# Kernel tuning notes

Measured on AMD Instinct MI355X. Metric: run time of the kernel, lower is better.

## Reference

```python
import jax, jax.numpy as jnp
import numpy as np

N = 65536
R = 9          # num_relations + 1
D_IN = 256
D_HID = 512
D_OUT = 256
N_HIDDEN = 2


def _xavier(key, shape):
    fan_out, fan_in = shape[-2], shape[-1]
    limit = np.sqrt(6.0 / (fan_in + fan_out))
    return jax.random.uniform(key, shape, jnp.float32, -limit, limit)


def setup_inputs() -> dict:
    key = jax.random.key(0)
    ks = jax.random.split(key, 12)
    inp = {
        "x": jax.random.normal(ks[0], (N, D_IN), jnp.float32),
        "edge_attr": jax.random.uniform(ks[1], (N, R), jnp.float32),
    }
    dims = [(D_HID, D_IN)] + [(D_HID, D_HID)] * N_HIDDEN + [(D_OUT, D_HID)]
    for i, (o, ii) in enumerate(dims):
        inp[f"W{i}"] = _xavier(ks[2 + 2 * i], (R, o, ii))
        inp[f"b{i}"] = _xavier(ks[3 + 2 * i], (R, o))
    return inp


def _linear_kg(x, edge_attr, W, b):
    # roi,ni,nr->no : relation-mixed linear per node
    y = jnp.einsum("roi,ni,nr->no", W, x, edge_attr)
    return y + edge_attr @ b


def reference(x, edge_attr, W0, b0, W1, b1, W2, b2, W3, b3):
    y = jax.nn.relu(_linear_kg(x, edge_attr, W0, b0))
    y = jax.nn.relu(_linear_kg(y, edge_attr, W1, b1))
    y = jax.nn.relu(_linear_kg(y, edge_attr, W2, b2))
    y = _linear_kg(y, edge_attr, W3, b3)
    return y
```

## Files before the change

### kernel.cpp

```cpp
#include <hip/hip_runtime.h>
#include <stdint.h>

using f32x4  = __attribute__((ext_vector_type(4))) float;
using bf16x8 = __attribute__((ext_vector_type(8))) __bf16;

#define GLOAD_LDS16(src, dst) __builtin_amdgcn_global_load_lds(                 \
    (const __attribute__((address_space(1))) void*)(src),                      \
    (__attribute__((address_space(3))) void*)(dst), 16, 0, 0)


__global__ void cvt_x_kernel(const float* __restrict__ x, __bf16* __restrict__ out) {
    const int u    = blockIdx.x * 256 + threadIdx.x;
    const int lane = u & 63;
    const int f    = (u >> 6) & 31;
    const int c    = (u >> 11) & 1;
    const int rb   = u >> 12;
    const int row  = rb * 128 + ((f >> 2) << 4) + (lane & 15);
    const int i    = c * 128 + ((f & 3) << 5) + ((lane >> 4) << 3);
    const float4 a = *(const float4*)(x + (size_t)row * 256 + i);
    const float4 b = *(const float4*)(x + (size_t)row * 256 + i + 4);
    bf16x8 pv;
    pv[0] = (__bf16)a.x; pv[1] = (__bf16)a.y; pv[2] = (__bf16)a.z; pv[3] = (__bf16)a.w;
    pv[4] = (__bf16)b.x; pv[5] = (__bf16)b.y; pv[6] = (__bf16)b.z; pv[7] = (__bf16)b.w;
    *(bf16x8*)(out + (size_t)u * 8) = pv;
}

template<int I, int O>
__global__ void prep_w_kernel(const float* __restrict__ W, __bf16* __restrict__ Bt) {
    constexpr int NCH = I >> 7;
    const int u    = blockIdx.x * 256 + threadIdx.x;
    const int r    = blockIdx.y;
    const int nb   = blockIdx.z;
    const int lane = u & 63;
    const int g    = (u >> 6) & 15;
    const int h    = (u >> 10) & 1;
    const int c    = u >> 11;
    const int mi   = g >> 1;
    const int ks   = (h << 1) + (g & 1);
    const int row  = nb * 128 + mi * 16 + (lane & 15);
    const int i    = c * 128 + ks * 32 + ((lane >> 4) << 3);
    const float* src = W + ((size_t)r * O + row) * I + i;
    const float4 a = *(const float4*)src;
    const float4 b = *(const float4*)(src + 4);
    bf16x8 pv;
    pv[0] = (__bf16)a.x; pv[1] = (__bf16)a.y; pv[2] = (__bf16)a.z; pv[3] = (__bf16)a.w;
    pv[4] = (__bf16)b.x; pv[5] = (__bf16)b.y; pv[6] = (__bf16)b.z; pv[7] = (__bf16)b.w;
    *(bf16x8*)(Bt + ((((size_t)nb * 9 + r) * NCH + c) * 2048 + (u & 2047)) * 8) = pv;
}

template<int O>
__global__ void prep_bias_kernel(const float* __restrict__ b, __bf16* __restrict__ BtB) {
    const int u    = blockIdx.x * 256 + threadIdx.x;
    const int nb   = u >> 10;
    const int q    = u & 1023;
    const int lane = q & 63;
    const int f    = q >> 6;
    const int row  = nb * 128 + ((f >> 1) << 4) + (lane & 15);
    const int kb   = ((f & 1) << 5) + ((lane >> 4) << 3);
    bf16x8 pv;
#pragma unroll
    for (int e = 0; e < 8; ++e) {
        const int k = kb + e;
        pv[e] = (k < 9) ? (__bf16)b[(size_t)k * O + row] : (__bf16)0.f;
    }
    *(bf16x8*)(BtB + (size_t)u * 8) = pv;
}

template<int I, int O, bool RELU, bool OUTF32>
__global__ __launch_bounds__(256, 2)
void kg_gemm(const __bf16* __restrict__ A, const float* __restrict__ E,
             const __bf16* __restrict__ Bt, const __bf16* __restrict__ BtB,
             void* __restrict__ Outv) {
    constexpr int NCH = I >> 7;
    constexpr int NBN = O >> 7;
    static_assert((I & 127) == 0 && (O & 127) == 0, "tile divisibility");

    __shared__ __align__(16) char lds[65536 + 4608];
    float* const ldsE = (float*)(lds + 65536);

    const int tid  = threadIdx.x;
    const int nwg  = gridDim.x;
    const int braw = blockIdx.x;
    const int bid  = (braw & 7) * (nwg >> 3) + (braw >> 3);
    const int rb   = bid / NBN;
    const int nb   = bid % NBN;
    const int bm0  = rb << 7;
    const int bn0  = nb << 7;
    const int lane = tid & 63;
    const int wid  = tid >> 6;
    const int wr   = (wid >> 1) << 6;
    const int wc   = (wid & 1) << 6;
    const int l15  = lane & 15;
    const int lq   = lane >> 4;

    if (tid < 128) {
        const float* e = E + (size_t)(bm0 + tid) * 9;
#pragma unroll
        for (int q = 0; q < 9; ++q) ldsE[q * 128 + tid] = e[q];
    }
    asm volatile("s_waitcnt lgkmcnt(0)" ::: "memory");
    __builtin_amdgcn_s_barrier();

    f32x4 acc[4][4];
#pragma unroll
    for (int m = 0; m < 4; ++m)
#pragma unroll
        for (int n = 0; n < 4; ++n)
            acc[m][n] = f32x4{0.f, 0.f, 0.f, 0.f};
    const f32x4 zero4 = {0.f, 0.f, 0.f, 0.f};

    const size_t Bbase = (size_t)nb * 9 * NCH * 2048;
    const __bf16* Arb  = A + (size_t)rb * NCH * 2048 * 8;
    const int afb = (wr >> 4) << 2;
    const int g0  = (wc >> 4) << 1;
    char* const wlds = lds + (wid << 14);

    auto stageW = [&](int r2, int c2, int h2) {
        const __bf16* src = Bt + (Bbase + ((size_t)r2 * NCH + c2) * 2048
                                  + (h2 << 10) + (g0 << 6)) * 8;
        char* dst = wlds + (h2 << 13);
#pragma unroll
        for (int it = 0; it < 8; ++it) {
            const int q = it * 64 + lane;
            GLOAD_LDS16(src + (size_t)q * 8, dst + q * 16);
        }
    };

    bf16x8 af[4][4];
    stageW(0, 0, 0); stageW(0, 0, 1);

#pragma unroll 1
    for (int c = 0; c < NCH; ++c) {
#pragma unroll 1
        for (int r = 0; r < 9; ++r) {
            f32x4 acc2[4][4];
#pragma unroll
            for (int h = 0; h < 2; ++h) {
                const bool first = (r == 0) && (h == 0);
                const bool lastC = (c == NCH - 1);
                if (first) {
                    const __bf16* Ab = Arb + (size_t)c * 2048 * 8;
#pragma unroll
                    for (int m = 0; m < 4; ++m)
#pragma unroll
                        for (int ks = 0; ks < 4; ++ks)
                            af[m][ks] = *(const bf16x8*)(Ab + ((size_t)((afb + (m << 2) + ks) << 6) + lane) * 8);
                    asm volatile("s_waitcnt vmcnt(24)" ::: "memory");
                } else if (lastC && r == 8 && h == 1) {
                    asm volatile("s_waitcnt vmcnt(0)" ::: "memory");
                } else {
                    asm volatile("s_waitcnt vmcnt(8)" ::: "memory");
                }
                __builtin_amdgcn_sched_barrier(0);
                const char* bp = wlds + (h << 13);
                bf16x8 bv[4][2];
#pragma unroll
                for (int n = 0; n < 4; ++n)
#pragma unroll
                    for (int j = 0; j < 2; ++j)
                        bv[n][j] = *(const bf16x8*)(bp + ((((n << 1) + j) << 6) + lane) * 16);
                asm volatile("s_waitcnt lgkmcnt(0)" ::: "memory");
                __builtin_amdgcn_sched_barrier(0);
                if (!(lastC && r == 8))
                    stageW((r < 8) ? r + 1 : 0, (r < 8) ? c : c + 1, h);
                if (first) asm volatile("s_waitcnt vmcnt(8)" ::: "memory");
                __builtin_amdgcn_sched_barrier(0);
                __builtin_amdgcn_s_setprio(1);
#pragma unroll
                for (int j = 0; j < 2; ++j)
#pragma unroll
                    for (int m = 0; m < 4; ++m)
#pragma unroll
                        for (int n = 0; n < 4; ++n)
                            acc2[m][n] = __builtin_amdgcn_mfma_f32_16x16x32_bf16(
                                af[m][(h << 1) + j], bv[n][j],
                                (h == 0 && j == 0) ? zero4 : acc2[m][n], 0, 0, 0);
                __builtin_amdgcn_s_setprio(0);
            }
#pragma unroll
            for (int m = 0; m < 4; ++m) {
                const f32x4 ev = *(const f32x4*)(ldsE + r * 128 + wr + m * 16 + lq * 4);
#pragma unroll
                for (int n = 0; n < 4; ++n)
#pragma unroll
                    for (int j = 0; j < 4; ++j)
                        acc[m][n][j] += ev[j] * acc2[m][n][j];
            }
        }
    }

    __syncthreads();
    {
        char* const bufB = lds;
        char* const bufA = lds + 16384;
#pragma unroll
        for (int rr = 0; rr < 4; ++rr) {
            const int q = rr * 256 + tid;
            GLOAD_LDS16(BtB + ((size_t)nb * 1024 + q) * 8, bufB + q * 16);
        }
#pragma unroll
        for (int rr = 0; rr < 4; ++rr) {
            const int q    = rr * 256 + tid;
            const int ln   = q & 63;
            const int f    = q >> 6;
            const int row  = ((f >> 1) << 4) + (ln & 15);
            const int kb   = ((f & 1) << 5) + ((ln >> 4) << 3);
            bf16x8 pv;
#pragma unroll
            for (int e8 = 0; e8 < 8; ++e8) {
                const int k = kb + e8;
                pv[e8] = (k < 9) ? (__bf16)ldsE[k * 128 + row] : (__bf16)0.f;
            }
            *(bf16x8*)(bufA + q * 16) = pv;
        }
        __syncthreads();
#pragma unroll
        for (int ks = 0; ks < 2; ++ks) {
            bf16x8 av[4], bv[4];
#pragma unroll
            for (int m = 0; m < 4; ++m)
                av[m] = *(const bf16x8*)(bufA + (((((wr >> 4) + m) * 2 + ks) << 6) + lane) * 16);
#pragma unroll
            for (int n = 0; n < 4; ++n)
                bv[n] = *(const bf16x8*)(bufB + (((((wc >> 4) + n) * 2 + ks) << 6) + lane) * 16);
#pragma unroll
            for (int m = 0; m < 4; ++m)
#pragma unroll
                for (int n = 0; n < 4; ++n)
                    acc[m][n] = __builtin_amdgcn_mfma_f32_16x16x32_bf16(
                        av[m], bv[n], acc[m][n], 0, 0, 0);
        }
    }

    if (OUTF32) {
        const int orow0 = bm0 + wr + lq * 4;
        const int ocol0 = bn0 + wc + l15;
#pragma unroll
        for (int m = 0; m < 4; ++m)
#pragma unroll
            for (int n = 0; n < 4; ++n)
#pragma unroll
                for (int j = 0; j < 4; ++j) {
                    float v = acc[m][n][j];
                    if (RELU) v = fmaxf(v, 0.f);
                    ((float*)Outv)[(size_t)(orow0 + m * 16 + j) * O + (ocol0 + n * 16)] = v;
                }
    } else {
        constexpr int NCHn = O >> 7;
        __bf16* outp = (__bf16*)Outv;
#pragma unroll
        for (int m = 0; m < 4; ++m) {
#pragma unroll
            for (int n = 0; n < 4; ++n) {
                const int col  = bn0 + wc + n * 16 + l15;
                const int c2   = col >> 7;
                const int f2   = (((wr >> 4) + m) << 2) + ((col >> 5) & 3);
                const int ln2  = ((col >> 3) & 3) * 16 + lq * 4;
                const size_t base =
                    (((size_t)rb * NCHn + c2) * 2048 + f2 * 64 + ln2) * 8 + (col & 7);
#pragma unroll
                for (int j = 0; j < 4; ++j) {
                    float v = acc[m][n][j];
                    if (RELU) v = fmaxf(v, 0.f);
                    outp[base + (size_t)j * 8] = (__bf16)v;
                }
            }
        }
    }
}

extern "C" void kernel_launch(void* const* d_in, const int* in_sizes, int n_in,
                              void* d_out, int out_size, void* d_ws, size_t ws_size,
                              hipStream_t stream) {
    const float* x  = (const float*)d_in[0];
    const float* E  = (const float*)d_in[1];
    const float* W0 = (const float*)d_in[2];
    const float* b0 = (const float*)d_in[3];
    const float* W1 = (const float*)d_in[4];
    const float* b1 = (const float*)d_in[5];
    const float* W2 = (const float*)d_in[6];
    const float* b2 = (const float*)d_in[7];
    const float* W3 = (const float*)d_in[8];
    const float* b3 = (const float*)d_in[9];

    char* ws = (char*)d_ws;
    const size_t actBytes = (size_t)65536 * 512 * 2;
    __bf16* actA = (__bf16*)ws;
    __bf16* actB = (__bf16*)(ws + actBytes);
    char* p = ws + 2 * actBytes;
    __bf16* Bt0 = (__bf16*)p; p += (size_t)4 * 9 * 2 * 2048 * 16;
    __bf16* Bt1 = (__bf16*)p; p += (size_t)4 * 9 * 4 * 2048 * 16;
    __bf16* Bt2 = (__bf16*)p; p += (size_t)4 * 9 * 4 * 2048 * 16;
    __bf16* Bt3 = (__bf16*)p; p += (size_t)2 * 9 * 4 * 2048 * 16;
    __bf16* BtB0 = (__bf16*)p; p += (size_t)4 * 1024 * 16;
    __bf16* BtB1 = (__bf16*)p; p += (size_t)4 * 1024 * 16;
    __bf16* BtB2 = (__bf16*)p; p += (size_t)4 * 1024 * 16;
    __bf16* BtB3 = (__bf16*)p; p += (size_t)2 * 1024 * 16;
    if (ws_size < (size_t)(p - ws)) return;

    cvt_x_kernel<<<dim3(8192), dim3(256), 0, stream>>>(x, actA);
    prep_w_kernel<256, 512><<<dim3(16, 9, 4), dim3(256), 0, stream>>>(W0, Bt0);
    prep_w_kernel<512, 512><<<dim3(32, 9, 4), dim3(256), 0, stream>>>(W1, Bt1);
    prep_w_kernel<512, 512><<<dim3(32, 9, 4), dim3(256), 0, stream>>>(W2, Bt2);
    prep_w_kernel<512, 256><<<dim3(32, 9, 2), dim3(256), 0, stream>>>(W3, Bt3);
    prep_bias_kernel<512><<<dim3(16), dim3(256), 0, stream>>>(b0, BtB0);
    prep_bias_kernel<512><<<dim3(16), dim3(256), 0, stream>>>(b1, BtB1);
    prep_bias_kernel<512><<<dim3(16), dim3(256), 0, stream>>>(b2, BtB2);
    prep_bias_kernel<256><<<dim3(8),  dim3(256), 0, stream>>>(b3, BtB3);

    kg_gemm<256, 512, true,  false><<<dim3(2048), dim3(256), 0, stream>>>(actA, E, Bt0, BtB0, actB);
    kg_gemm<512, 512, true,  false><<<dim3(2048), dim3(256), 0, stream>>>(actB, E, Bt1, BtB1, actA);
    kg_gemm<512, 512, true,  false><<<dim3(2048), dim3(256), 0, stream>>>(actA, E, Bt2, BtB2, actB);
    kg_gemm<512, 256, false, true ><<<dim3(1024), dim3(256), 0, stream>>>(actB, E, Bt3, BtB3, d_out);
}
```

Before: 970.8 us.

## Fold per-relation scaling into each K-half and restart weight staging per chunk

Drops the acc2 intermediate that held the relation-r partial product across both K-halves. Each half's MFMA result is now scaled by the edge_attr coefficients and added into the main accumulator right away, which cuts register use at the cost of doing the VALU scaling twice per relation. Weight staging no longer prefetches across chunk boundaries: the A fragments and the first relation's weights are loaded at the start of each chunk. The s_setprio hints are removed, and the MFMA issue order is reorganised into independent chains of four. This may open a pipeline bubble at every chunk start in exchange for lower register pressure and simpler waitcnt logic.

```diff
diff --git a/kernel.cpp b/kernel.cpp
--- a/kernel.cpp
+++ b/kernel.cpp
@@ -112,12 +112,12 @@
     const size_t Bbase = (size_t)nb * 9 * NCH * 2048;
     const __bf16* Arb  = A + (size_t)rb * NCH * 2048 * 8;
     const int afb = (wr >> 4) << 2;
-    const int g0  = (wc >> 4) << 1;
+    const int G0  = (wid & 1) << 3;
     char* const wlds = lds + (wid << 14);
 
     auto stageW = [&](int r2, int c2, int h2) {
         const __bf16* src = Bt + (Bbase + ((size_t)r2 * NCH + c2) * 2048
-                                  + (h2 << 10) + (g0 << 6)) * 8;
+                                  + (h2 << 10) + (G0 << 6)) * 8;
         char* dst = wlds + (h2 << 13);
 #pragma unroll
         for (int it = 0; it < 8; ++it) {
@@ -127,30 +127,29 @@
     };
 
     bf16x8 af[4][4];
-    stageW(0, 0, 0); stageW(0, 0, 1);
 
 #pragma unroll 1
     for (int c = 0; c < NCH; ++c) {
+        asm volatile("s_waitcnt lgkmcnt(0)" ::: "memory");
+        __builtin_amdgcn_sched_barrier(0);
+        {
+            const __bf16* Ab = Arb + (size_t)c * 2048 * 8;
+#pragma unroll
+            for (int m = 0; m < 4; ++m)
+#pragma unroll
+                for (int ks = 0; ks < 4; ++ks)
+                    af[m][ks] = *(const bf16x8*)(Ab + ((size_t)((afb + (m << 2) + ks) << 6) + lane) * 8);
+        }
+        stageW(0, c, 0);
+        stageW(0, c, 1);
+
 #pragma unroll 1
         for (int r = 0; r < 9; ++r) {
-            f32x4 acc2[4][4];
 #pragma unroll
             for (int h = 0; h < 2; ++h) {
-                const bool first = (r == 0) && (h == 0);
-                const bool lastC = (c == NCH - 1);
-                if (first) {
-                    const __bf16* Ab = Arb + (size_t)c * 2048 * 8;
-#pragma unroll
-                    for (int m = 0; m < 4; ++m)
-#pragma unroll
-                        for (int ks = 0; ks < 4; ++ks)
-                            af[m][ks] = *(const bf16x8*)(Ab + ((size_t)((afb + (m << 2) + ks) << 6) + lane) * 8);
-                    asm volatile("s_waitcnt vmcnt(24)" ::: "memory");
-                } else if (lastC && r == 8 && h == 1) {
-                    asm volatile("s_waitcnt vmcnt(0)" ::: "memory");
-                } else {
-                    asm volatile("s_waitcnt vmcnt(8)" ::: "memory");
-                }
+                const int s = 2 * r + h;
+                if (s < 17) asm volatile("s_waitcnt vmcnt(8)" ::: "memory");
+                else        asm volatile("s_waitcnt vmcnt(0)" ::: "memory");
                 __builtin_amdgcn_sched_barrier(0);
                 const char* bp = wlds + (h << 13);
                 bf16x8 bv[4][2];
@@ -159,32 +158,33 @@
 #pragma unroll
                     for (int j = 0; j < 2; ++j)
                         bv[n][j] = *(const bf16x8*)(bp + ((((n << 1) + j) << 6) + lane) * 16);
-                asm volatile("s_waitcnt lgkmcnt(0)" ::: "memory");
-                __builtin_amdgcn_sched_barrier(0);
-                if (!(lastC && r == 8))
-                    stageW((r < 8) ? r + 1 : 0, (r < 8) ? c : c + 1, h);
-                if (first) asm volatile("s_waitcnt vmcnt(8)" ::: "memory");
-                __builtin_amdgcn_sched_barrier(0);
-                __builtin_amdgcn_s_setprio(1);
-#pragma unroll
-                for (int j = 0; j < 2; ++j)
-#pragma unroll
-                    for (int m = 0; m < 4; ++m)
-#pragma unroll
-                        for (int n = 0; n < 4; ++n)
-                            acc2[m][n] = __builtin_amdgcn_mfma_f32_16x16x32_bf16(
-                                af[m][(h << 1) + j], bv[n][j],
-                                (h == 0 && j == 0) ? zero4 : acc2[m][n], 0, 0, 0);
-                __builtin_amdgcn_s_setprio(0);
-            }
-#pragma unroll
-            for (int m = 0; m < 4; ++m) {
-                const f32x4 ev = *(const f32x4*)(ldsE + r * 128 + wr + m * 16 + lq * 4);
-#pragma unroll
-                for (int n = 0; n < 4; ++n)
-#pragma unroll
-                    for (int j = 0; j < 4; ++j)
-                        acc[m][n][j] += ev[j] * acc2[m][n][j];
+                f32x4 ev[4];
+#pragma unroll
+                for (int m = 0; m < 4; ++m)
+                    ev[m] = *(const f32x4*)(ldsE + r * 128 + wr + m * 16 + lq * 4);
+#pragma unroll
+                for (int n = 0; n < 4; ++n) {
+                    f32x4 t0 = __builtin_amdgcn_mfma_f32_16x16x32_bf16(af[0][2*h], bv[n][0], zero4, 0, 0, 0);
+                    f32x4 t1 = __builtin_amdgcn_mfma_f32_16x16x32_bf16(af[1][2*h], bv[n][0], zero4, 0, 0, 0);
+                    f32x4 t2 = __builtin_amdgcn_mfma_f32_16x16x32_bf16(af[2][2*h], bv[n][0], zero4, 0, 0, 0);
+                    f32x4 t3 = __builtin_amdgcn_mfma_f32_16x16x32_bf16(af[3][2*h], bv[n][0], zero4, 0, 0, 0);
+                    t0 = __builtin_amdgcn_mfma_f32_16x16x32_bf16(af[0][2*h+1], bv[n][1], t0, 0, 0, 0);
+                    t1 = __builtin_amdgcn_mfma_f32_16x16x32_bf16(af[1][2*h+1], bv[n][1], t1, 0, 0, 0);
+                    t2 = __builtin_amdgcn_mfma_f32_16x16x32_bf16(af[2][2*h+1], bv[n][1], t2, 0, 0, 0);
+                    t3 = __builtin_amdgcn_mfma_f32_16x16x32_bf16(af[3][2*h+1], bv[n][1], t3, 0, 0, 0);
+#pragma unroll
+                    for (int j = 0; j < 4; ++j) {
+                        acc[0][n][j] += ev[0][j] * t0[j];
+                        acc[1][n][j] += ev[1][j] * t1[j];
+                        acc[2][n][j] += ev[2][j] * t2[j];
+                        acc[3][n][j] += ev[3][j] * t3[j];
+                    }
+                }
+                if (s + 2 <= 17) {
+                    asm volatile("s_waitcnt lgkmcnt(0)" ::: "memory");
+                    __builtin_amdgcn_sched_barrier(0);
+                    stageW(r + 1, c, h);
+                }
             }
         }
     }
```

After: 2.045 ms. 111% more time.
